# Performance work log

Hardware: AMD Instinct MI355X
Metric: run time of the kernel (lower is better)

The kernel has to match this reference:

```python
import jax, jax.numpy as jnp
import numpy as np

B, T, U = 4, 256, 128
EH, PH, JH, V = 1024, 640, 640, 1024


def setup_inputs() -> dict:
    key = jax.random.key(0)
    ks = jax.random.split(key, 8)
    s_e = 1.0 / np.sqrt(EH)
    s_p = 1.0 / np.sqrt(PH)
    s_j = 1.0 / np.sqrt(JH)
    return {
        "enc": jax.random.normal(ks[0], (B, EH, T), jnp.float32),
        "dec": jax.random.normal(ks[1], (B, PH, U), jnp.float32),
        "W_enc": jax.random.uniform(ks[2], (JH, EH), jnp.float32, -s_e, s_e),
        "b_enc": jax.random.uniform(ks[3], (JH,), jnp.float32, -s_e, s_e),
        "W_pred": jax.random.uniform(ks[4], (JH, PH), jnp.float32, -s_p, s_p),
        "b_pred": jax.random.uniform(ks[5], (JH,), jnp.float32, -s_p, s_p),
        "W_out": jax.random.uniform(ks[6], (V, JH), jnp.float32, -s_j, s_j),
        "b_out": jax.random.uniform(ks[7], (V,), jnp.float32, -s_j, s_j),
    }


def reference(enc, dec, W_enc, b_enc, W_pred, b_pred, W_out, b_out):
    # enc: [B, EH, T], dec: [B, PH, U]  (channels-first, as in torch forward)
    # enc projection -> [B, T, JH] (transpose fused into einsum)
    e = jnp.einsum('bht,jh->btj', enc, W_enc) + b_enc
    # pred projection -> [B, U, JH]
    p = jnp.einsum('bhu,jh->buj', dec, W_pred) + b_pred
    # broadcast add -> [B, T, U, JH], ReLU, output projection -> [B, T, U, V]
    h = jax.nn.relu(e[:, :, None, :] + p[:, None, :, :])
    logits = jnp.einsum('btuj,vj->btuv', h, W_out) + b_out
    return jax.nn.log_softmax(logits, axis=-1)
```

## Files before the change

### kernel.cpp

```cpp
#include <hip/hip_runtime.h>
#include <hip/hip_bf16.h>
#include <stdint.h>

#define B_ 4
#define T_ 256
#define U_ 128
#define EH_ 1024
#define PH_ 640
#define JH_ 640
#define V_ 1024
#define KT_ 20

typedef short bf16x8 __attribute__((ext_vector_type(8)));
typedef float f32x4 __attribute__((ext_vector_type(4)));
typedef unsigned short u16;

__device__ __forceinline__ u16 f2bf(float f) {
  union { float f; uint32_t u; } v;
  v.f = f;
  uint32_t u = v.u;
  return (u16)((u + 0x7FFFu + ((u >> 16) & 1u)) >> 16);
}

__device__ __forceinline__ uint32_t cvt2(float lo, float hi) {
  uint32_t r;
  asm("v_cvt_pk_bf16_f32 %0, %1, %2" : "=v"(r) : "v"(lo), "v"(hi));
  return r;
}

#define LGKM0  asm volatile("s_waitcnt lgkmcnt(0)" ::: "memory")

__global__ void k_transpose_cvt(const float* __restrict__ in, u16* __restrict__ out,
                                int H, int W) {
  __shared__ float tile[32][33];
  int b = blockIdx.z;
  int h0 = blockIdx.y * 32, w0 = blockIdx.x * 32;
  const float* pin = in + (size_t)b * H * W;
  u16* pout = out + (size_t)b * H * W;
  int lw = threadIdx.x & 31, lh = threadIdx.x >> 5;
#pragma unroll
  for (int i = 0; i < 4; i++) {
    int h = lh + i * 8;
    tile[h][lw] = pin[(size_t)(h0 + h) * W + (w0 + lw)];
  }
  __syncthreads();
#pragma unroll
  for (int i = 0; i < 4; i++) {
    int w = lh + i * 8;
    pout[(size_t)(w0 + w) * H + (h0 + lw)] = f2bf(tile[lw][w]);
  }
}

__global__ void k_prep_w(const float* __restrict__ We, const float* __restrict__ Wp,
                         const float* __restrict__ Wo,
                         u16* __restrict__ WeB, u16* __restrict__ WpB,
                         u16* __restrict__ Wpk) {
  int s = blockIdx.x * 256 + threadIdx.x;
  if (s < 163840) {
    int idx = s * 4;
    float4 v = *(const float4*)(We + idx);
    ushort4 o;
    o.x = f2bf(v.x); o.y = f2bf(v.y); o.z = f2bf(v.z); o.w = f2bf(v.w);
    *(ushort4*)(WeB + idx) = o;
  } else if (s < 266240) {
    int idx = (s - 163840) * 4;
    float4 v = *(const float4*)(Wp + idx);
    ushort4 o;
    o.x = f2bf(v.x); o.y = f2bf(v.y); o.z = f2bf(v.z); o.w = f2bf(v.w);
    *(ushort4*)(WpB + idx) = o;
  } else {
    int q = s - 266240;
    int c = q & 1023;
    int g = (q >> 10) & 3;
    int t = q >> 12;
    const float* src = Wo + (size_t)c * JH_ + t * 32 + g * 8;
    float4 a = *(const float4*)src;
    float4 b2 = *(const float4*)(src + 4);
    ushort4 lo, hi;
    lo.x = f2bf(a.x);  lo.y = f2bf(a.y);  lo.z = f2bf(a.z);  lo.w = f2bf(a.w);
    hi.x = f2bf(b2.x); hi.y = f2bf(b2.y); hi.z = f2bf(b2.z); hi.w = f2bf(b2.w);
    u16* d = Wpk + (size_t)q * 8;
    *(ushort4*)d = lo;
    *(ushort4*)(d + 4) = hi;
  }
}

__global__ void k_proj_gemm(const u16* __restrict__ A, const u16* __restrict__ Bm,
                            const float* __restrict__ bias, float* __restrict__ C,
                            int K, int N, size_t strideA, size_t strideC) {
  __shared__ __align__(16) u16 sA[64 * 64];
  __shared__ __align__(16) u16 sB[64 * 64];
  int bb = blockIdx.z;
  const u16* Ab = A + (size_t)bb * strideA;
  float* Cb = C + (size_t)bb * strideC;
  int m0 = blockIdx.x * 64, n0 = blockIdx.y * 64;
  int tid = threadIdx.x;
  int lane = tid & 63, wid = tid >> 6;

  f32x4 acc[2][2] = {};
  for (int kk = 0; kk < K; kk += 64) {
#pragma unroll
    for (int i = 0; i < 2; i++) {
      int c = tid + i * 256;
      int r = c >> 3, kc = c & 7;
      int s = (r << 3) | (kc ^ (r & 7));
      *(bf16x8*)(sA + s * 8) = *(const bf16x8*)(Ab + (size_t)(m0 + r) * K + kk + kc * 8);
      *(bf16x8*)(sB + s * 8) = *(const bf16x8*)(Bm + (size_t)(n0 + r) * K + kk + kc * 8);
    }
    __syncthreads();
    int wr = (wid >> 1) * 32, wc = (wid & 1) * 32;
    int lr = lane & 15, lk = lane >> 4;
#pragma unroll
    for (int ki = 0; ki < 2; ki++) {
      bf16x8 af[2], bq[2];
#pragma unroll
      for (int mf = 0; mf < 2; mf++) {
        int r = wr + mf * 16 + lr;
        int kc = ki * 4 + lk;
        int s = (r << 3) | (kc ^ (r & 7));
        af[mf] = *(const bf16x8*)(sA + s * 8);
      }
#pragma unroll
      for (int nf = 0; nf < 2; nf++) {
        int r = wc + nf * 16 + lr;
        int kc = ki * 4 + lk;
        int s = (r << 3) | (kc ^ (r & 7));
        bq[nf] = *(const bf16x8*)(sB + s * 8);
      }
#pragma unroll
      for (int mf = 0; mf < 2; mf++)
#pragma unroll
        for (int nf = 0; nf < 2; nf++)
          acc[mf][nf] = __builtin_amdgcn_mfma_f32_16x16x32_bf16(af[mf], bq[nf], acc[mf][nf], 0, 0, 0);
    }
    __syncthreads();
  }
  int wr = (wid >> 1) * 32, wc = (wid & 1) * 32;
  int lr = lane & 15, lq = lane >> 4;
#pragma unroll
  for (int nf = 0; nf < 2; nf++) {
    int n = n0 + wc + nf * 16 + lr;
    float bv = bias[n];
#pragma unroll
    for (int mf = 0; mf < 2; mf++) {
#pragma unroll
      for (int r = 0; r < 4; r++) {
        int m = m0 + wr + mf * 16 + lq * 4 + r;
        Cb[(size_t)m * N + n] = acc[mf][nf][r] + bv;
      }
    }
  }
}

__global__ void k_pack_p2(const float* __restrict__ pBuf, float* __restrict__ pPk) {
  int s = blockIdx.x * 256 + threadIdx.x;
  int bh = s / 10240;
  int rem = s - bh * 10240;
  int g4 = rem >> 6;
  int r = rem & 63;
  int b = bh >> 1, half = bh & 1;
  const float* src = pBuf + ((size_t)(b * 128 + half * 64 + r)) * JH_ + g4 * 4;
  float4 v = *(const float4*)src;
  *(float4*)(pPk + (size_t)s * 4) = v;
}

__global__ __launch_bounds__(512)
void k_fused7(const float* __restrict__ e, const float* __restrict__ pPk,
              const u16* __restrict__ Wpk, const float* __restrict__ bout,
              float* __restrict__ out) {
  __shared__ __align__(16) u16 sA[2][4096];
  __shared__ __align__(16) float sE[JH_];
  __shared__ float redm[512];
  __shared__ float reds[512];

  int bid = blockIdx.x;
  int btile = bid >> 1, half = bid & 1, b = btile >> 8;
  int tid = threadIdx.x, lane = tid & 63, wn = tid >> 6;
  int lr = lane & 15, lk = lane >> 4;

  const float* eRow = e + (size_t)btile * JH_;
  const float* pPbase = pPk + ((size_t)(b * 2 + half) * 40960) + wn * 256 + lane * 4;
  const u16* wB = Wpk + ((size_t)lk * 1024 + wn * 128 + lr) * 8;
  float* outB = out + ((size_t)btile * U_ + half * 64) * V_;

  int awr = (wn >> 1) * 512 + lane * 8 + (wn & 1) * 4;

  f32x4 acc[4][8] = {};
  bf16x8 bq[2][8];

  auto loadB = [&](int t, bf16x8* d) {
#pragma unroll
    for (int nf = 0; nf < 8; nf++)
      d[nf] = *(const bf16x8*)(wB + (size_t)t * 32768 + nf * 128);
  };
  auto loadp = [&](int t) { return *(const float4*)(pPbase + t * 2048); };
  auto build = [&](int slot, int tin, int t, float4 pv) {
    float4 ev = *(const float4*)(&sE[t * 32 + wn * 4]);
    uint2 w;
    w.x = cvt2(fmaxf(pv.x + ev.x, 0.f), fmaxf(pv.y + ev.y, 0.f));
    w.y = cvt2(fmaxf(pv.z + ev.z, 0.f), fmaxf(pv.w + ev.w, 0.f));
    *(uint2*)(&sA[slot][tin * 2048 + awr]) = w;
  };

  loadB(0, bq[0]);
  for (int i = tid; i < JH_; i += 512) sE[i] = eRow[i];
  float4 p0  = loadp(0);
  float4 p1  = loadp(1);
  float4 pcA = loadp(2);
  float4 pcB = loadp(3);
  float4 pnA = p0, pnB = p0;
  LGKM0;
  __builtin_amdgcn_s_barrier();
  build(0, 0, 0, p0);
  build(0, 1, 1, p1);
  LGKM0;
  __builtin_amdgcn_s_barrier();

#pragma unroll
  for (int t = 0; t < KT_; t++) {
    if (t + 1 < KT_) loadB(t + 1, bq[(t + 1) & 1]);
    if ((t & 1) == 0) {
      if (t + 4 < KT_) { pnA = loadp(t + 4); pnB = loadp(t + 5); }
      if (t + 2 < KT_) {
        int q1 = ((t >> 1) + 1) & 1;
        build(q1, 0, t + 2, pcA);
        build(q1, 1, t + 3, pcB);
      }
    }
    const u16* Ab = &sA[(t >> 1) & 1][(t & 1) * 2048 + lk * 512];
    bf16x8 af[4];
#pragma unroll
    for (int mf = 0; mf < 4; mf++)
      af[mf] = *(const bf16x8*)(Ab + (mf * 16 + lr) * 8);
    __builtin_amdgcn_s_setprio(1);
#pragma unroll
    for (int mf = 0; mf < 4; mf++)
#pragma unroll
      for (int nf = 0; nf < 8; nf++)
        acc[mf][nf] = __builtin_amdgcn_mfma_f32_16x16x32_bf16(bq[t & 1][nf], af[mf], acc[mf][nf], 0, 0, 0);
    __builtin_amdgcn_s_setprio(0);
    if ((t & 1) && t + 1 < KT_) {
      pcA = pnA; pcB = pnB;
      LGKM0;
      __builtin_amdgcn_s_barrier();
    }
  }

#pragma unroll
  for (int nf = 0; nf < 8; nf++) {
    f32x4 bv = *(const f32x4*)(bout + wn * 128 + nf * 16 + lk * 4);
#pragma unroll
    for (int mf = 0; mf < 4; mf++) acc[mf][nf] += bv;
  }
  float gm[4], lsv[4];
#pragma unroll
  for (int mf = 0; mf < 4; mf++) {
    float m = acc[mf][0][0];
#pragma unroll
    for (int nf = 0; nf < 8; nf++)
#pragma unroll
      for (int j = 0; j < 4; j++) m = fmaxf(m, acc[mf][nf][j]);
    m = fmaxf(m, __shfl_xor(m, 16, 64));
    m = fmaxf(m, __shfl_xor(m, 32, 64));
    gm[mf] = m;
  }
  if (lane < 16) {
#pragma unroll
    for (int mf = 0; mf < 4; mf++) redm[(mf * 16 + lr) * 8 + wn] = gm[mf];
  }
  __syncthreads();
#pragma unroll
  for (int mf = 0; mf < 4; mf++) {
    float m = redm[(mf * 16 + lr) * 8];
#pragma unroll
    for (int w = 1; w < 8; w++) m = fmaxf(m, redm[(mf * 16 + lr) * 8 + w]);
    gm[mf] = m;
  }
#pragma unroll
  for (int mf = 0; mf < 4; mf++) {
    float s = 0.f;
#pragma unroll
    for (int nf = 0; nf < 8; nf++)
#pragma unroll
      for (int j = 0; j < 4; j++) s += __expf(acc[mf][nf][j] - gm[mf]);
    s += __shfl_xor(s, 16, 64);
    s += __shfl_xor(s, 32, 64);
    lsv[mf] = s;
  }
  if (lane < 16) {
#pragma unroll
    for (int mf = 0; mf < 4; mf++) reds[(mf * 16 + lr) * 8 + wn] = lsv[mf];
  }
  __syncthreads();
#pragma unroll
  for (int mf = 0; mf < 4; mf++) {
    float s = reds[(mf * 16 + lr) * 8];
#pragma unroll
    for (int w = 1; w < 8; w++) s += reds[(mf * 16 + lr) * 8 + w];
    lsv[mf] = gm[mf] + __logf(s);
  }

#pragma unroll
  for (int mf = 0; mf < 4; mf++) {
    float* orow = outB + (size_t)(mf * 16 + lr) * V_ + wn * 128 + lk * 4;
#pragma unroll
    for (int nf = 0; nf < 8; nf++) {
      f32x4 v = acc[mf][nf] - lsv[mf];
      *(f32x4*)(orow + nf * 16) = v;
    }
  }
}

extern "C" void kernel_launch(void* const* d_in, const int* in_sizes, int n_in,
                              void* d_out, int out_size, void* d_ws, size_t ws_size,
                              hipStream_t stream) {
  const float* enc    = (const float*)d_in[0];
  const float* dec    = (const float*)d_in[1];
  const float* W_enc  = (const float*)d_in[2];
  const float* b_enc  = (const float*)d_in[3];
  const float* W_pred = (const float*)d_in[4];
  const float* b_pred = (const float*)d_in[5];
  const float* W_out  = (const float*)d_in[6];
  const float* b_out  = (const float*)d_in[7];
  float* out = (float*)d_out;

  char* ws = (char*)d_ws;
  size_t off = 0;
  auto alloc = [&](size_t bytes) {
    void* pp = ws + off;
    off = (off + bytes + 255) & ~(size_t)255;
    return pp;
  };
  u16* encT   = (u16*)alloc((size_t)B_ * T_ * EH_ * 2);
  u16* decT   = (u16*)alloc((size_t)B_ * U_ * PH_ * 2);
  u16* WencB  = (u16*)alloc((size_t)JH_ * EH_ * 2);
  u16* WpredB = (u16*)alloc((size_t)JH_ * PH_ * 2);
  u16* Wpk    = (u16*)alloc((size_t)KT_ * 32768 * 2);
  float* eBuf = (float*)alloc((size_t)B_ * T_ * JH_ * 4);
  float* pBuf = (float*)alloc((size_t)B_ * U_ * JH_ * 4);
  float* pPk  = (float*)alloc((size_t)81920 * 4 * 4);

  k_transpose_cvt<<<dim3(T_ / 32, EH_ / 32, B_), 256, 0, stream>>>(enc, encT, EH_, T_);
  k_transpose_cvt<<<dim3(U_ / 32, PH_ / 32, B_), 256, 0, stream>>>(dec, decT, PH_, U_);
  k_prep_w<<<1360, 256, 0, stream>>>(W_enc, W_pred, W_out, WencB, WpredB, Wpk);
  k_proj_gemm<<<dim3(T_ / 64, JH_ / 64, B_), 256, 0, stream>>>(
      encT, WencB, b_enc, eBuf, EH_, JH_, (size_t)T_ * EH_, (size_t)T_ * JH_);
  k_proj_gemm<<<dim3(U_ / 64, JH_ / 64, B_), 256, 0, stream>>>(
      decT, WpredB, b_pred, pBuf, PH_, JH_, (size_t)U_ * PH_, (size_t)U_ * JH_);
  k_pack_p2<<<320, 256, 0, stream>>>(pBuf, pPk);

  k_fused7<<<B_ * T_ * 2, 512, 0, stream>>>(eBuf, pPk, Wpk, b_out, out);
}
```

Baseline: 276.1 us.

## Process both U halves per block and prefetch second half during epilogue

Halves the grid so each block handles both 64-row halves of U for one (b,t) row, looping twice over the K pipeline. The second half's W and p loads are issued before the first half's output stores, with a scheduling barrier placed so the stores overlap with the prefetch. This amortizes block launch and sE loading and hides pipeline fill latency, but it halves the number of blocks and so risks lower occupancy and less latency hiding across the GPU.

```diff
diff --git a/kernel.cpp b/kernel.cpp
--- a/kernel.cpp
+++ b/kernel.cpp
@@ -29,6 +29,7 @@
 }
 
 #define LGKM0  asm volatile("s_waitcnt lgkmcnt(0)" ::: "memory")
+#define SCHEDB __builtin_amdgcn_sched_barrier(0)
 
 __global__ void k_transpose_cvt(const float* __restrict__ in, u16* __restrict__ out,
                                 int H, int W) {
@@ -165,7 +166,7 @@
 }
 
 __global__ __launch_bounds__(512)
-void k_fused7(const float* __restrict__ e, const float* __restrict__ pPk,
+void k_fused8(const float* __restrict__ e, const float* __restrict__ pPk,
               const u16* __restrict__ Wpk, const float* __restrict__ bout,
               float* __restrict__ out) {
   __shared__ __align__(16) u16 sA[2][4096];
@@ -174,18 +175,18 @@
   __shared__ float reds[512];
 
   int bid = blockIdx.x;
-  int btile = bid >> 1, half = bid & 1, b = btile >> 8;
+  int btile = bid, b = btile >> 8;
   int tid = threadIdx.x, lane = tid & 63, wn = tid >> 6;
   int lr = lane & 15, lk = lane >> 4;
 
   const float* eRow = e + (size_t)btile * JH_;
-  const float* pPbase = pPk + ((size_t)(b * 2 + half) * 40960) + wn * 256 + lane * 4;
   const u16* wB = Wpk + ((size_t)lk * 1024 + wn * 128 + lr) * 8;
-  float* outB = out + ((size_t)btile * U_ + half * 64) * V_;
 
   int awr = (wn >> 1) * 512 + lane * 8 + (wn & 1) * 4;
 
-  f32x4 acc[4][8] = {};
+  const float* pPbase = pPk + ((size_t)(b * 2) * 40960) + wn * 256 + lane * 4;
+  float* outB = out + ((size_t)btile * U_) * V_;
+
   bf16x8 bq[2][8];
 
   auto loadB = [&](int t, bf16x8* d) {
@@ -216,97 +217,120 @@
   LGKM0;
   __builtin_amdgcn_s_barrier();
 
-#pragma unroll
-  for (int t = 0; t < KT_; t++) {
-    if (t + 1 < KT_) loadB(t + 1, bq[(t + 1) & 1]);
-    if ((t & 1) == 0) {
-      if (t + 4 < KT_) { pnA = loadp(t + 4); pnB = loadp(t + 5); }
-      if (t + 2 < KT_) {
-        int q1 = ((t >> 1) + 1) & 1;
-        build(q1, 0, t + 2, pcA);
-        build(q1, 1, t + 3, pcB);
-      }
-    }
-    const u16* Ab = &sA[(t >> 1) & 1][(t & 1) * 2048 + lk * 512];
-    bf16x8 af[4];
-#pragma unroll
-    for (int mf = 0; mf < 4; mf++)
-      af[mf] = *(const bf16x8*)(Ab + (mf * 16 + lr) * 8);
-    __builtin_amdgcn_s_setprio(1);
-#pragma unroll
-    for (int mf = 0; mf < 4; mf++)
+#pragma unroll 1
+  for (int hu = 0; hu < 2; hu++) {
+    f32x4 acc[4][8] = {};
+#pragma unroll
+    for (int t = 0; t < KT_; t++) {
+      if (t + 1 < KT_) loadB(t + 1, bq[(t + 1) & 1]);
+      if ((t & 1) == 0) {
+        if (t + 4 < KT_) { pnA = loadp(t + 4); pnB = loadp(t + 5); }
+        if (t + 2 < KT_) {
+          int q1 = ((t >> 1) + 1) & 1;
+          build(q1, 0, t + 2, pcA);
+          build(q1, 1, t + 3, pcB);
+        }
+      }
+      const u16* Ab = &sA[(t >> 1) & 1][(t & 1) * 2048 + lk * 512];
+      bf16x8 af[4];
+#pragma unroll
+      for (int mf = 0; mf < 4; mf++)
+        af[mf] = *(const bf16x8*)(Ab + (mf * 16 + lr) * 8);
+      __builtin_amdgcn_s_setprio(1);
+#pragma unroll
+      for (int mf = 0; mf < 4; mf++)
+#pragma unroll
+        for (int nf = 0; nf < 8; nf++)
+          acc[mf][nf] = __builtin_amdgcn_mfma_f32_16x16x32_bf16(bq[t & 1][nf], af[mf], acc[mf][nf], 0, 0, 0);
+      __builtin_amdgcn_s_setprio(0);
+      if ((t & 1) && t + 1 < KT_) {
+        pcA = pnA; pcB = pnB;
+        LGKM0;
+        __builtin_amdgcn_s_barrier();
+      }
+    }
+
+#pragma unroll
+    for (int nf = 0; nf < 8; nf++) {
+      f32x4 bv = *(const f32x4*)(bout + wn * 128 + nf * 16 + lk * 4);
+#pragma unroll
+      for (int mf = 0; mf < 4; mf++) acc[mf][nf] += bv;
+    }
+    float gm[4], lsv[4];
+#pragma unroll
+    for (int mf = 0; mf < 4; mf++) {
+      float m = acc[mf][0][0];
 #pragma unroll
       for (int nf = 0; nf < 8; nf++)
-        acc[mf][nf] = __builtin_amdgcn_mfma_f32_16x16x32_bf16(bq[t & 1][nf], af[mf], acc[mf][nf], 0, 0, 0);
-    __builtin_amdgcn_s_setprio(0);
-    if ((t & 1) && t + 1 < KT_) {
-      pcA = pnA; pcB = pnB;
+#pragma unroll
+        for (int j = 0; j < 4; j++) m = fmaxf(m, acc[mf][nf][j]);
+      m = fmaxf(m, __shfl_xor(m, 16, 64));
+      m = fmaxf(m, __shfl_xor(m, 32, 64));
+      gm[mf] = m;
+    }
+    if (lane < 16) {
+#pragma unroll
+      for (int mf = 0; mf < 4; mf++) redm[(mf * 16 + lr) * 8 + wn] = gm[mf];
+    }
+    __syncthreads();
+#pragma unroll
+    for (int mf = 0; mf < 4; mf++) {
+      float m = redm[(mf * 16 + lr) * 8];
+#pragma unroll
+      for (int w = 1; w < 8; w++) m = fmaxf(m, redm[(mf * 16 + lr) * 8 + w]);
+      gm[mf] = m;
+    }
+#pragma unroll
+    for (int mf = 0; mf < 4; mf++) {
+      float s = 0.f;
+#pragma unroll
+      for (int nf = 0; nf < 8; nf++)
+#pragma unroll
+        for (int j = 0; j < 4; j++) s += __expf(acc[mf][nf][j] - gm[mf]);
+      s += __shfl_xor(s, 16, 64);
+      s += __shfl_xor(s, 32, 64);
+      lsv[mf] = s;
+    }
+    if (lane < 16) {
+#pragma unroll
+      for (int mf = 0; mf < 4; mf++) reds[(mf * 16 + lr) * 8 + wn] = lsv[mf];
+    }
+    __syncthreads();
+#pragma unroll
+    for (int mf = 0; mf < 4; mf++) {
+      float s = reds[(mf * 16 + lr) * 8];
+#pragma unroll
+      for (int w = 1; w < 8; w++) s += reds[(mf * 16 + lr) * 8 + w];
+      lsv[mf] = gm[mf] + __logf(s);
+    }
+
+    float* outC = outB;
+    if (hu == 0) {
+      pPbase = pPk + ((size_t)(b * 2 + 1) * 40960) + wn * 256 + lane * 4;
+      outB = out + ((size_t)btile * U_ + 64) * V_;
+      loadB(0, bq[0]);
+      p0  = loadp(0);
+      p1  = loadp(1);
+      pcA = loadp(2);
+      pcB = loadp(3);
+    }
+    SCHEDB;
+
+#pragma unroll
+    for (int mf = 0; mf < 4; mf++) {
+      float* orow = outC + (size_t)(mf * 16 + lr) * V_ + wn * 128 + lk * 4;
+#pragma unroll
+      for (int nf = 0; nf < 8; nf++) {
+        f32x4 v = acc[mf][nf] - lsv[mf];
+        *(f32x4*)(orow + nf * 16) = v;
+      }
+    }
+
+    if (hu == 0) {
+      build(0, 0, 0, p0);
+      build(0, 1, 1, p1);
       LGKM0;
       __builtin_amdgcn_s_barrier();
-    }
-  }
-
-#pragma unroll
-  for (int nf = 0; nf < 8; nf++) {
-    f32x4 bv = *(const f32x4*)(bout + wn * 128 + nf * 16 + lk * 4);
-#pragma unroll
-    for (int mf = 0; mf < 4; mf++) acc[mf][nf] += bv;
-  }
-  float gm[4], lsv[4];
-#pragma unroll
-  for (int mf = 0; mf < 4; mf++) {
-    float m = acc[mf][0][0];
-#pragma unroll
-    for (int nf = 0; nf < 8; nf++)
-#pragma unroll
-      for (int j = 0; j < 4; j++) m = fmaxf(m, acc[mf][nf][j]);
-    m = fmaxf(m, __shfl_xor(m, 16, 64));
-    m = fmaxf(m, __shfl_xor(m, 32, 64));
-    gm[mf] = m;
-  }
-  if (lane < 16) {
-#pragma unroll
-    for (int mf = 0; mf < 4; mf++) redm[(mf * 16 + lr) * 8 + wn] = gm[mf];
-  }
-  __syncthreads();
-#pragma unroll
-  for (int mf = 0; mf < 4; mf++) {
-    float m = redm[(mf * 16 + lr) * 8];
-#pragma unroll
-    for (int w = 1; w < 8; w++) m = fmaxf(m, redm[(mf * 16 + lr) * 8 + w]);
-    gm[mf] = m;
-  }
-#pragma unroll
-  for (int mf = 0; mf < 4; mf++) {
-    float s = 0.f;
-#pragma unroll
-    for (int nf = 0; nf < 8; nf++)
-#pragma unroll
-      for (int j = 0; j < 4; j++) s += __expf(acc[mf][nf][j] - gm[mf]);
-    s += __shfl_xor(s, 16, 64);
-    s += __shfl_xor(s, 32, 64);
-    lsv[mf] = s;
-  }
-  if (lane < 16) {
-#pragma unroll
-    for (int mf = 0; mf < 4; mf++) reds[(mf * 16 + lr) * 8 + wn] = lsv[mf];
-  }
-  __syncthreads();
-#pragma unroll
-  for (int mf = 0; mf < 4; mf++) {
-    float s = reds[(mf * 16 + lr) * 8];
-#pragma unroll
-    for (int w = 1; w < 8; w++) s += reds[(mf * 16 + lr) * 8 + w];
-    lsv[mf] = gm[mf] + __logf(s);
-  }
-
-#pragma unroll
-  for (int mf = 0; mf < 4; mf++) {
-    float* orow = outB + (size_t)(mf * 16 + lr) * V_ + wn * 128 + lk * 4;
-#pragma unroll
-    for (int nf = 0; nf < 8; nf++) {
-      f32x4 v = acc[mf][nf] - lsv[mf];
-      *(f32x4*)(orow + nf * 16) = v;
     }
   }
 }
@@ -349,5 +373,5 @@
       decT, WpredB, b_pred, pBuf, PH_, JH_, (size_t)U_ * PH_, (size_t)U_ * JH_);
   k_pack_p2<<<320, 256, 0, stream>>>(pBuf, pPk);
 
-  k_fused7<<<B_ * T_ * 2, 512, 0, stream>>>(eBuf, pPk, Wpk, b_out, out);
-}
+  k_fused8<<<B_ * T_, 512, 0, stream>>>(eBuf, pPk, Wpk, b_out, out);
+}
```

Measured after the change: 932.0 us. +237.5%, slower.
